# Kernel optimization log

Hardware: AMD Instinct MI355X
Metric: run time of the kernel (lower is better)

The kernel has to match this reference:

```python
import jax, jax.numpy as jnp
import numpy as np

N = 50000      # nodes
D = 128        # feature dim
NNZ = 800000   # edges (avg degree 16)
M = 30         # Chebyshev order

def setup_inputs() -> dict:
    key = jax.random.key(0)
    k1, k2, k3, k4, k5 = jax.random.split(key, 5)
    rows = jax.random.randint(k1, (NNZ,), 0, N)
    cols = jax.random.randint(k2, (NNZ,), 0, N)
    # scale so row sums (Gershgorin bound on spectral radius) stay ~< 1,
    # mimicking a rescaled Laplacian required for a stable Chebyshev recurrence
    vals = jax.random.uniform(k3, (NNZ,), dtype=jnp.float32) * (0.5 / 16.0)
    X = jax.random.normal(k4, (N, D), dtype=jnp.float32)
    coeffs = jax.random.normal(k5, (M,), dtype=jnp.float32)
    return {"rows": rows, "cols": cols, "vals": vals, "X": X, "coeffs": coeffs}

def _spmm(rows, cols, vals, X, n):
    # y[r] += vals[e] * X[c]  for each edge e=(r,c): sparse L @ X
    return jax.ops.segment_sum(vals[:, None] * X[cols], rows, num_segments=n)

def reference(rows, cols, vals, X, coeffs):
    n = X.shape[0]
    T0 = X                                   # T_0 = X
    T1 = _spmm(rows, cols, vals, X, n)       # T_1 = L @ X
    acc = coeffs[0] * T0 + coeffs[1] * T1
    def step(carry, ck):
        T0, T1, acc = carry
        Tk = 2.0 * _spmm(rows, cols, vals, T1, n) - T0   # T_k = 2 L T_{k-1} - T_{k-2}
        return (T1, Tk, acc + ck * Tk), None
    (_, _, acc), _ = jax.lax.scan(step, (T0, T1, acc), coeffs[2:])
    return acc
```

## Files before the change

### kernel.cpp

```cpp
#include <hip/hip_runtime.h>
#include <hip/hip_fp16.h>

#define FD 128
#define RPB 4


__global__ void zero_i32(int* __restrict__ p, int n) {
  int i = blockIdx.x * blockDim.x + threadIdx.x;
  if (i < n) p[i] = 0;
}

__global__ void hist_kernel(const int* __restrict__ rows, int* __restrict__ cnt, int nnz) {
  int i = blockIdx.x * blockDim.x + threadIdx.x;
  if (i < nnz) atomicAdd(&cnt[rows[i]], 1);
}

__global__ void block_reduce(const int* __restrict__ cnt, int* __restrict__ bsum, int n) {
  __shared__ int sm[256];
  int i = blockIdx.x * 256 + threadIdx.x;
  sm[threadIdx.x] = (i < n) ? cnt[i] : 0;
  __syncthreads();
  for (int off = 128; off > 0; off >>= 1) {
    if (threadIdx.x < off) sm[threadIdx.x] += sm[threadIdx.x + off];
    __syncthreads();
  }
  if (threadIdx.x == 0) bsum[blockIdx.x] = sm[0];
}

__global__ void scan_bsum(const int* __restrict__ bsum, int* __restrict__ bpre, int nb) {
  __shared__ int sm[1024];
  const int tid = threadIdx.x;
  sm[tid] = (tid < nb) ? bsum[tid] : 0;
  __syncthreads();
  for (int off = 1; off < 1024; off <<= 1) {
    int t = (tid >= off) ? sm[tid - off] : 0;
    __syncthreads();
    sm[tid] += t;
    __syncthreads();
  }
  if (tid < nb) bpre[tid] = (tid == 0) ? 0 : sm[tid - 1];
}

__global__ void block_scan(const int* __restrict__ cnt, const int* __restrict__ bpre,
                           int* __restrict__ row_ptr, int n) {
  __shared__ int sm[256];
  const int tid = threadIdx.x;
  int i = blockIdx.x * 256 + tid;
  sm[tid] = (i < n) ? cnt[i] : 0;
  __syncthreads();
  for (int off = 1; off < 256; off <<= 1) {
    int t = (tid >= off) ? sm[tid - off] : 0;
    __syncthreads();
    sm[tid] += t;
    __syncthreads();
  }
  if (i < n) row_ptr[i + 1] = sm[tid] + bpre[blockIdx.x];
  if (i == 0) row_ptr[0] = 0;
}

__global__ void copy_i32(const int* __restrict__ src, int* __restrict__ dst, int n) {
  int i = blockIdx.x * blockDim.x + threadIdx.x;
  if (i < n) dst[i] = src[i];
}

__global__ void scatter_kernel(const int* __restrict__ rows, const int* __restrict__ cols,
                               const float* __restrict__ vals, int* __restrict__ fill,
                               int2* __restrict__ pk, int nnz) {
  int i = blockIdx.x * blockDim.x + threadIdx.x;
  if (i < nnz) {
    int r = rows[i];
    int pos = atomicAdd(&fill[r], 1);
    pk[pos] = make_int2(cols[i], __float_as_int(vals[i]));
  }
}

__global__ void f32_to_f16(const float* __restrict__ src, __half* __restrict__ dst, int n4) {
  int i = blockIdx.x * blockDim.x + threadIdx.x;
  if (i < n4) {
    float4 v = ((const float4*)src)[i];
    __half2* d = (__half2*)dst + 2 * (size_t)i;
    d[0] = __floats2half2_rn(v.x, v.y);
    d[1] = __floats2half2_rn(v.z, v.w);
  }
}

__global__ void clen_first(const __half2* __restrict__ Xh, __half2* __restrict__ b,
                           const float* __restrict__ coeffs, int kidx, int n2) {
  int i = blockIdx.x * blockDim.x + threadIdx.x;
  if (i < n2) {
    const float c = coeffs[kidx];
    float2 x = __half22float2(Xh[i]);
    b[i] = __floats2half2_rn(c * x.x, c * x.y);
  }
}


__device__ __forceinline__ void fma_edge(const __half* __restrict__ T, int c, float v,
                                         int fl, float2 acc[4]) {
  uint4 raw = ((const uint4*)(T + (size_t)c * FD))[fl];
  const __half2* h = (const __half2*)&raw;
  float2 x0 = __half22float2(h[0]);
  float2 x1 = __half22float2(h[1]);
  float2 x2 = __half22float2(h[2]);
  float2 x3 = __half22float2(h[3]);
  acc[0].x = fmaf(v, x0.x, acc[0].x); acc[0].y = fmaf(v, x0.y, acc[0].y);
  acc[1].x = fmaf(v, x1.x, acc[1].x); acc[1].y = fmaf(v, x1.y, acc[1].y);
  acc[2].x = fmaf(v, x2.x, acc[2].x); acc[2].y = fmaf(v, x2.y, acc[2].y);
  acc[3].x = fmaf(v, x3.x, acc[3].x); acc[3].y = fmaf(v, x3.y, acc[3].y);
}

__device__ __forceinline__ void gather_row(const int* __restrict__ rp,
                                           const int2* __restrict__ pk,
                                           const __half* __restrict__ T,
                                           int r, int sub, int fl, float2 acc[4]) {
  int e = rp[r];
  const int end = rp[r + 1];
  for (; e + 8 <= end; e += 8) {
    int2 cv0 = pk[e + sub];
    int2 cv1 = pk[e + 4 + sub];
    fma_edge(T, cv0.x, __int_as_float(cv0.y), fl, acc);
    fma_edge(T, cv1.x, __int_as_float(cv1.y), fl, acc);
  }
  if (e + 4 <= end) {
    int2 cv = pk[e + sub];
    fma_edge(T, cv.x, __int_as_float(cv.y), fl, acc);
    e += 4;
  }
  if (e < end) {
    int idx = e + sub;
    int2 cv = pk[min(idx, end - 1)];
    float v = (idx < end) ? __int_as_float(cv.y) : 0.f;
    fma_edge(T, cv.x, v, fl, acc);
  }
}

__device__ __forceinline__ void reduce_subs(float2 acc[4]) {
#pragma unroll
  for (int m = 16; m < 64; m <<= 1) {
#pragma unroll
    for (int q = 0; q < 4; ++q) {
      acc[q].x += __shfl_xor(acc[q].x, m, 64);
      acc[q].y += __shfl_xor(acc[q].y, m, 64);
    }
  }
}


__global__ __launch_bounds__(256) void clen_step(
    const int* __restrict__ rp, const int2* __restrict__ pk,
    const __half* __restrict__ src, const __half* __restrict__ Xh, __half* pd,
    const float* __restrict__ coeffs, int k, int has_p, int n) {
  const int lane = threadIdx.x & 63;
  const int sub = lane >> 4, fl = lane & 15;
  const int r = blockIdx.x * RPB + (threadIdx.x >> 6);
  if (r >= n) return;
  float2 acc[4] = {{0.f,0.f},{0.f,0.f},{0.f,0.f},{0.f,0.f}};
  gather_row(rp, pk, src, r, sub, fl, acc);
  reduce_subs(acc);
  if (sub == 0) {
    const float ck = coeffs[k];
    uint4 xr = ((const uint4*)(Xh + (size_t)r * FD))[fl];
    const __half2* xh = (const __half2*)&xr;
    float2 p[4] = {{0.f,0.f},{0.f,0.f},{0.f,0.f},{0.f,0.f}};
    if (has_p) {
      uint4 pr = ((const uint4*)(pd + (size_t)r * FD))[fl];
      const __half2* ph = (const __half2*)&pr;
#pragma unroll
      for (int q = 0; q < 4; ++q) p[q] = __half22float2(ph[q]);
    }
    uint4 orr;
    __half2* oh = (__half2*)&orr;
#pragma unroll
    for (int q = 0; q < 4; ++q) {
      float2 x = __half22float2(xh[q]);
      float tx = fmaf(2.f, acc[q].x, fmaf(ck, x.x, -p[q].x));
      float ty = fmaf(2.f, acc[q].y, fmaf(ck, x.y, -p[q].y));
      oh[q] = __floats2half2_rn(tx, ty);
    }
    ((uint4*)(pd + (size_t)r * FD))[fl] = orr;
  }
}

__global__ __launch_bounds__(256) void clen_final(
    const int* __restrict__ rp, const int2* __restrict__ pk,
    const __half* __restrict__ b1, const __half* __restrict__ b2,
    const float* __restrict__ X, float* __restrict__ out,
    const float* __restrict__ coeffs, int n) {
  const int lane = threadIdx.x & 63;
  const int sub = lane >> 4, fl = lane & 15;
  const int r = blockIdx.x * RPB + (threadIdx.x >> 6);
  if (r >= n) return;
  float2 acc[4] = {{0.f,0.f},{0.f,0.f},{0.f,0.f},{0.f,0.f}};
  gather_row(rp, pk, b1, r, sub, fl, acc);
  reduce_subs(acc);
  if (sub == 0) {
    const float c0 = coeffs[0];
    uint4 pr = ((const uint4*)(b2 + (size_t)r * FD))[fl];
    const __half2* ph = (const __half2*)&pr;
    float4 x0 = ((const float4*)(X + (size_t)r * FD))[fl * 2];
    float4 x1 = ((const float4*)(X + (size_t)r * FD))[fl * 2 + 1];
    float2 p0 = __half22float2(ph[0]), p1 = __half22float2(ph[1]);
    float2 p2 = __half22float2(ph[2]), p3 = __half22float2(ph[3]);
    float4 o0, o1;
    o0.x = fmaf(c0, x0.x, acc[0].x - p0.x);
    o0.y = fmaf(c0, x0.y, acc[0].y - p0.y);
    o0.z = fmaf(c0, x0.z, acc[1].x - p1.x);
    o0.w = fmaf(c0, x0.w, acc[1].y - p1.y);
    o1.x = fmaf(c0, x1.x, acc[2].x - p2.x);
    o1.y = fmaf(c0, x1.y, acc[2].y - p2.y);
    o1.z = fmaf(c0, x1.z, acc[3].x - p3.x);
    o1.w = fmaf(c0, x1.w, acc[3].y - p3.y);
    ((float4*)(out + (size_t)r * FD))[fl * 2] = o0;
    ((float4*)(out + (size_t)r * FD))[fl * 2 + 1] = o1;
  }
}


extern "C" void kernel_launch(void* const* d_in, const int* in_sizes, int n_in,
                              void* d_out, int out_size, void* d_ws, size_t ws_size,
                              hipStream_t stream) {
  const int* rows = (const int*)d_in[0];
  const int* cols = (const int*)d_in[1];
  const float* vals = (const float*)d_in[2];
  const float* X = (const float*)d_in[3];
  const float* coeffs = (const float*)d_in[4];
  float* out = (float*)d_out;

  const int nnz = in_sizes[0];
  const int n = in_sizes[3] / FD;
  const int M = in_sizes[4];

  auto align_up = [](size_t x) { return (x + 255) & ~(size_t)255; };
  char* w = (char*)d_ws;
  size_t off = 0;
  int* row_ptr = (int*)(w + off); off = align_up(off + (size_t)(n + 1) * 4);
  int* row_fill = (int*)(w + off); off = align_up(off + (size_t)n * 4);
  int* bsum = (int*)(w + off); off = align_up(off + 1024 * 4);
  int* bpre = (int*)(w + off); off = align_up(off + 1024 * 4);
  int2* pk = (int2*)(w + off); off = align_up(off + (size_t)nnz * 8);
  __half* Xh = (__half*)(w + off); off = align_up(off + (size_t)n * FD * 2);
  __half* buf0 = (__half*)(w + off); off = align_up(off + (size_t)n * FD * 2);
  __half* buf1 = (__half*)(w + off); off = align_up(off + (size_t)n * FD * 2);
  __half* bufs[2] = {buf0, buf1};
  (void)ws_size;

  const int B = 256;
  const int gN = (n + B - 1) / B;
  const int gE = (nnz + B - 1) / B;
  const int gS = (n + RPB - 1) / RPB;
  const int n4 = n * FD / 4;
  const int gC = (n4 + B - 1) / B;
  const int n2 = n * FD / 2;
  const int gH = (n2 + B - 1) / B;

  zero_i32<<<gN, B, 0, stream>>>(row_fill, n);
  hist_kernel<<<gE, B, 0, stream>>>(rows, row_fill, nnz);
  block_reduce<<<gN, B, 0, stream>>>(row_fill, bsum, n);
  scan_bsum<<<1, 1024, 0, stream>>>(bsum, bpre, gN);
  block_scan<<<gN, B, 0, stream>>>(row_fill, bpre, row_ptr, n);
  copy_i32<<<gN, B, 0, stream>>>(row_ptr, row_fill, n);
  scatter_kernel<<<gE, B, 0, stream>>>(rows, cols, vals, row_fill, pk, nnz);
  f32_to_f16<<<gC, B, 0, stream>>>(X, Xh, n4);

  clen_first<<<gH, B, 0, stream>>>((const __half2*)Xh, (__half2*)bufs[(M - 1) & 1],
                                   coeffs, M - 1, n2);
  for (int k = M - 2; k >= 1; --k) {
    clen_step<<<gS, B, 0, stream>>>(row_ptr, pk, bufs[(k + 1) & 1], Xh, bufs[k & 1],
                                    coeffs, k, (k < M - 2) ? 1 : 0, n);
  }
  clen_final<<<gS, B, 0, stream>>>(row_ptr, pk, bufs[1], bufs[0], X, out, coeffs, n);
}
```

Before: 1.149 ms.

## Batch gather loads for ILP and fold first Clenshaw term into step kernels

The per-row gather now issues up to eight rounds of index loads, then all the matching feature-row loads, and only then the FMAs, so many memory requests are in flight at once. A tail loop handles rows with more than 32 edges. The edge array gets 32 zero-padded slots so reads past the end stay safe. The separate clen_first kernel is dropped: Clenshaw's linearity lets the first two step launches use scaled coefficients directly on X. This saves one elementwise pass over the feature matrix, at the cost of more registers for the batched loads.

```diff
diff --git a/kernel.cpp b/kernel.cpp
--- a/kernel.cpp
+++ b/kernel.cpp
@@ -67,6 +67,7 @@
                                const float* __restrict__ vals, int* __restrict__ fill,
                                int2* __restrict__ pk, int nnz) {
   int i = blockIdx.x * blockDim.x + threadIdx.x;
+  if (i < 32) pk[nnz + i] = make_int2(0, 0);
   if (i < nnz) {
     int r = rows[i];
     int pos = atomicAdd(&fill[r], 1);
@@ -84,20 +85,8 @@
   }
 }
 
-__global__ void clen_first(const __half2* __restrict__ Xh, __half2* __restrict__ b,
-                           const float* __restrict__ coeffs, int kidx, int n2) {
-  int i = blockIdx.x * blockDim.x + threadIdx.x;
-  if (i < n2) {
-    const float c = coeffs[kidx];
-    float2 x = __half22float2(Xh[i]);
-    b[i] = __floats2half2_rn(c * x.x, c * x.y);
-  }
-}
-
-
-__device__ __forceinline__ void fma_edge(const __half* __restrict__ T, int c, float v,
-                                         int fl, float2 acc[4]) {
-  uint4 raw = ((const uint4*)(T + (size_t)c * FD))[fl];
+
+__device__ __forceinline__ void fma4(const uint4& raw, float v, float2 acc[4]) {
   const __half2* h = (const __half2*)&raw;
   float2 x0 = __half22float2(h[0]);
   float2 x1 = __half22float2(h[1]);
@@ -113,24 +102,30 @@
                                            const int2* __restrict__ pk,
                                            const __half* __restrict__ T,
                                            int r, int sub, int fl, float2 acc[4]) {
-  int e = rp[r];
+  const int e0 = rp[r];
   const int end = rp[r + 1];
-  for (; e + 8 <= end; e += 8) {
-    int2 cv0 = pk[e + sub];
-    int2 cv1 = pk[e + 4 + sub];
-    fma_edge(T, cv0.x, __int_as_float(cv0.y), fl, acc);
-    fma_edge(T, cv1.x, __int_as_float(cv1.y), fl, acc);
-  }
-  if (e + 4 <= end) {
-    int2 cv = pk[e + sub];
-    fma_edge(T, cv.x, __int_as_float(cv.y), fl, acc);
-    e += 4;
-  }
-  if (e < end) {
+  const int d = end - e0;
+  const int rounds = min((d + 3) >> 2, 8);
+  int2 cv[8];
+  uint4 xr[8];
+#pragma unroll
+  for (int j = 0; j < 8; ++j)
+    if (j < rounds) cv[j] = pk[e0 + 4 * j + sub];
+#pragma unroll
+  for (int j = 0; j < 8; ++j)
+    if (j < rounds) xr[j] = ((const uint4*)(T + (size_t)cv[j].x * FD))[fl];
+#pragma unroll
+  for (int j = 0; j < 8; ++j)
+    if (j < rounds) {
+      float v = (4 * j + sub < d) ? __int_as_float(cv[j].y) : 0.f;
+      fma4(xr[j], v, acc);
+    }
+  for (int e = e0 + 32; e < end; e += 4) {
     int idx = e + sub;
-    int2 cv = pk[min(idx, end - 1)];
-    float v = (idx < end) ? __int_as_float(cv.y) : 0.f;
-    fma_edge(T, cv.x, v, fl, acc);
+    int2 c = pk[idx];
+    float v = (idx < end) ? __int_as_float(c.y) : 0.f;
+    uint4 x = ((const uint4*)(T + (size_t)c.x * FD))[fl];
+    fma4(x, v, acc);
   }
 }
 
@@ -149,7 +144,7 @@
 __global__ __launch_bounds__(256) void clen_step(
     const int* __restrict__ rp, const int2* __restrict__ pk,
     const __half* __restrict__ src, const __half* __restrict__ Xh, __half* pd,
-    const float* __restrict__ coeffs, int k, int has_p, int n) {
+    const float* __restrict__ coeffs, int k, int flags, int M, int n) {
   const int lane = threadIdx.x & 63;
   const int sub = lane >> 4, fl = lane & 15;
   const int r = blockIdx.x * RPB + (threadIdx.x >> 6);
@@ -158,11 +153,13 @@
   gather_row(rp, pk, src, r, sub, fl, acc);
   reduce_subs(acc);
   if (sub == 0) {
-    const float ck = coeffs[k];
+    float ck = coeffs[k];
+    if (flags & 2) ck -= coeffs[M - 1];
+    const float g2 = (flags & 4) ? 2.f * coeffs[M - 1] : 2.f;
     uint4 xr = ((const uint4*)(Xh + (size_t)r * FD))[fl];
     const __half2* xh = (const __half2*)&xr;
     float2 p[4] = {{0.f,0.f},{0.f,0.f},{0.f,0.f},{0.f,0.f}};
-    if (has_p) {
+    if (flags & 1) {
       uint4 pr = ((const uint4*)(pd + (size_t)r * FD))[fl];
       const __half2* ph = (const __half2*)&pr;
 #pragma unroll
@@ -173,8 +170,8 @@
 #pragma unroll
     for (int q = 0; q < 4; ++q) {
       float2 x = __half22float2(xh[q]);
-      float tx = fmaf(2.f, acc[q].x, fmaf(ck, x.x, -p[q].x));
-      float ty = fmaf(2.f, acc[q].y, fmaf(ck, x.y, -p[q].y));
+      float tx = fmaf(g2, acc[q].x, fmaf(ck, x.x, -p[q].x));
+      float ty = fmaf(g2, acc[q].y, fmaf(ck, x.y, -p[q].y));
       oh[q] = __floats2half2_rn(tx, ty);
     }
     ((uint4*)(pd + (size_t)r * FD))[fl] = orr;
@@ -237,7 +234,7 @@
   int* row_fill = (int*)(w + off); off = align_up(off + (size_t)n * 4);
   int* bsum = (int*)(w + off); off = align_up(off + 1024 * 4);
   int* bpre = (int*)(w + off); off = align_up(off + 1024 * 4);
-  int2* pk = (int2*)(w + off); off = align_up(off + (size_t)nnz * 8);
+  int2* pk = (int2*)(w + off); off = align_up(off + ((size_t)nnz + 32) * 8);
   __half* Xh = (__half*)(w + off); off = align_up(off + (size_t)n * FD * 2);
   __half* buf0 = (__half*)(w + off); off = align_up(off + (size_t)n * FD * 2);
   __half* buf1 = (__half*)(w + off); off = align_up(off + (size_t)n * FD * 2);
@@ -250,8 +247,6 @@
   const int gS = (n + RPB - 1) / RPB;
   const int n4 = n * FD / 4;
   const int gC = (n4 + B - 1) / B;
-  const int n2 = n * FD / 2;
-  const int gH = (n2 + B - 1) / B;
 
   zero_i32<<<gN, B, 0, stream>>>(row_fill, n);
   hist_kernel<<<gE, B, 0, stream>>>(rows, row_fill, nnz);
@@ -262,11 +257,13 @@
   scatter_kernel<<<gE, B, 0, stream>>>(rows, cols, vals, row_fill, pk, nnz);
   f32_to_f16<<<gC, B, 0, stream>>>(X, Xh, n4);
 
-  clen_first<<<gH, B, 0, stream>>>((const __half2*)Xh, (__half2*)bufs[(M - 1) & 1],
-                                   coeffs, M - 1, n2);
-  for (int k = M - 2; k >= 1; --k) {
+  clen_step<<<gS, B, 0, stream>>>(row_ptr, pk, Xh, Xh, bufs[(M - 2) & 1],
+                                  coeffs, M - 2, 4, M, n);
+  clen_step<<<gS, B, 0, stream>>>(row_ptr, pk, bufs[(M - 2) & 1], Xh, bufs[(M - 3) & 1],
+                                  coeffs, M - 3, 2, M, n);
+  for (int k = M - 4; k >= 1; --k) {
     clen_step<<<gS, B, 0, stream>>>(row_ptr, pk, bufs[(k + 1) & 1], Xh, bufs[k & 1],
-                                    coeffs, k, (k < M - 2) ? 1 : 0, n);
+                                    coeffs, k, 1, M, n);
   }
   clen_final<<<gS, B, 0, stream>>>(row_ptr, pk, bufs[1], bufs[0], X, out, coeffs, n);
 }
```

Result: slower. 1.210 ms (+5.3%).
